# Kernel tuning notes

Measured on AMD Instinct MI355X. Metric: run time of the kernel, lower is better.

Reference implementation:

```python
import jax, jax.numpy as jnp
import numpy as np

N = 20000          # nodes
E = 320000         # edges (avg degree 16)
HID = 256          # hidden_size
HEADS = 8          # num_heads
HD = HID // HEADS  # head_dim = 32


def setup_inputs() -> dict:
    key = jax.random.key(0)
    ks = jax.random.split(key, 12)
    scale = 1.0 / np.sqrt(HID).astype(np.float32)
    def lin_w(k):
        return jax.random.normal(k, (HID, HID), jnp.float32) * scale
    def lin_b(k):
        return jax.random.normal(k, (HID,), jnp.float32) * 0.01
    return {
        "h":   jax.random.normal(ks[0], (N, HID), jnp.float32),
        "Wq": lin_w(ks[1]), "bq": lin_b(ks[2]),
        "Wk": lin_w(ks[3]), "bk": lin_b(ks[4]),
        "Wv": lin_w(ks[5]), "bv": lin_b(ks[6]),
        "Wo": lin_w(ks[7]), "bo": lin_b(ks[8]),
        "rows": jax.random.randint(ks[9],  (E,), 0, N),  # dst/query node of each edge
        "cols": jax.random.randint(ks[10], (E,), 0, N),  # src/key node of each edge
    }


def reference(h, Wq, bq, Wk, bk, Wv, bv, Wo, bo, rows, cols):
    n = h.shape[0]
    scaling = HD ** (-0.5)
    # projections; reshape exactly as torch: (N, head_dim, num_heads)
    q = ((h @ Wq) + bq).reshape(n, HD, HEADS) * scaling
    k = ((h @ Wk) + bk).reshape(n, HD, HEADS)
    v = ((h @ Wv) + bv).reshape(n, HD, HEADS)
    # bsddmm: per-edge, per-head score s[e,h] = sum_d q[rows[e],d,h] * k[cols[e],d,h]
    s = jnp.einsum("edh,edh->eh", q[rows], k[cols])  # [E, HEADS]
    # sparse row-wise softmax (over each row's edges)
    m = jax.ops.segment_max(s, rows, num_segments=n)          # [N, HEADS]
    e = jnp.exp(s - m[rows])                                   # [E, HEADS]
    z = jax.ops.segment_sum(e, rows, num_segments=n)           # [N, HEADS]
    attn = e / z[rows]                                          # [E, HEADS]
    # bspmm: out[i,d,h] = sum_{e: rows[e]=i} attn[e,h] * v[cols[e],d,h]
    out = jax.ops.segment_sum(attn[:, None, :] * v[cols], rows, num_segments=n)  # [N, HD, HEADS]
    return out.reshape(n, -1) @ Wo + bo
```

## Files before the change

kernel.cpp:

```cpp
#include <hip/hip_runtime.h>
#include <hip/hip_bf16.h>
#include <math.h>

#define NNODES 20000
#define NEDGES 320000

using f32x4 = __attribute__((ext_vector_type(4))) float;
using s16x8 = __attribute__((ext_vector_type(8))) short;
using u16x8 = __attribute__((ext_vector_type(8))) unsigned short;

__device__ __forceinline__ float bf2f(unsigned short u) {
    union { unsigned int i; float f; } c; c.i = ((unsigned int)u) << 16; return c.f;
}
__device__ __forceinline__ unsigned short f2bf(float f) {
    __hip_bfloat16 h = __float2bfloat16(f);
    return *reinterpret_cast<unsigned short*>(&h);
}

__global__ __launch_bounds__(256) void prep_hist_k(
    const float* __restrict__ Wq, const float* __restrict__ bq,
    const float* __restrict__ Wk, const float* __restrict__ bk,
    const float* __restrict__ Wv, const float* __restrict__ bv,
    const float* __restrict__ Wo, const int* __restrict__ rows,
    unsigned short* __restrict__ wt, float* __restrict__ bp,
    int* __restrict__ counts)
{
    const int gid = blockIdx.x * 256 + threadIdx.x;
    const float SC = 0.17677669529663687f;
    if (gid < 262144) {
        const int mat = gid >> 16, r = gid & 65535;
        if (mat < 3) {
            const int k = r >> 8, c = r & 255;
            const int n_old = ((c & 31) << 3) | (c >> 5);
            const float* W = (mat == 0) ? Wq : (mat == 1) ? Wk : Wv;
            float val = W[k * 256 + n_old];
            if (mat == 0) val *= SC;
            wt[mat * 65536 + c * 256 + k] = f2bf(val);
        } else {
            const int c = r >> 8, n = r & 255;
            const int n_old = ((c & 31) << 3) | (c >> 5);
            wt[3 * 65536 + n * 256 + c] = f2bf(Wo[n_old * 256 + n]);
        }
    } else if (gid < 262912) {
        const int idx = gid - 262144;
        const int mat = idx >> 8, c = idx & 255;
        const int n_old = ((c & 31) << 3) | (c >> 5);
        const float* b = (mat == 0) ? bq : (mat == 1) ? bk : bv;
        float val = b[n_old];
        if (mat == 0) val *= SC;
        bp[mat * 256 + c] = val;
    } else if (gid < 262912 + NEDGES) {
        atomicAdd(&counts[rows[gid - 262912]], 1);
    }
}

__global__ __launch_bounds__(1024) void scan_k(const int* __restrict__ counts,
                                               int* __restrict__ row_start)
{
    __shared__ int wsum[16];
    __shared__ int s_carry;
    const int t = threadIdx.x, lane = t & 63, w = t >> 6;
    if (t == 0) { s_carry = 0; row_start[0] = 0; }
    __syncthreads();
    for (int base = 0; base < NNODES; base += 4096) {
        int c[4]; int s4 = 0;
        #pragma unroll
        for (int j = 0; j < 4; ++j) {
            const int idx = base + t * 4 + j;
            c[j] = (idx < NNODES) ? counts[idx] : 0;
            s4 += c[j];
        }
        int incl = s4;
        #pragma unroll
        for (int off = 1; off < 64; off <<= 1) {
            const int y = __shfl_up(incl, off);
            if (lane >= off) incl += y;
        }
        if (lane == 63) wsum[w] = incl;
        __syncthreads();
        int prev = 0;
        for (int i = 0; i < w; ++i) prev += wsum[i];
        int total = 0;
        #pragma unroll
        for (int i = 0; i < 16; ++i) total += wsum[i];
        int run = s_carry + prev + incl - s4;
        #pragma unroll
        for (int j = 0; j < 4; ++j) {
            const int idx = base + t * 4 + j;
            run += c[j];
            if (idx < NNODES) row_start[idx + 1] = run;
        }
        __syncthreads();
        if (t == 0) s_carry += total;
        __syncthreads();
    }
}

__global__ void scatter_k(const int* __restrict__ rows, const int* __restrict__ cols,
                          const int* __restrict__ row_start, int* __restrict__ cursor,
                          int* __restrict__ cols_sorted)
{
    const int i = blockIdx.x * blockDim.x + threadIdx.x;
    if (i < NEDGES) {
        const int r = rows[i];
        const int pos = row_start[r] + atomicAdd(&cursor[r], 1);
        cols_sorted[pos] = cols[i];
    }
}

__global__ __launch_bounds__(256) void qkv_mfma_k(
    const float* __restrict__ h,
    const unsigned short* __restrict__ wt, const float* __restrict__ bp,
    unsigned short* __restrict__ qo, unsigned short* __restrict__ kv)
{
    const int bm = blockIdx.x * 128;
    const int mat = blockIdx.y >> 1;
    const int bn = (blockIdx.y & 1) * 128;
    const unsigned short* W = wt + mat * 65536;
    const float* bias = bp + mat * 256;

    __shared__ __align__(16) unsigned short As[128][40];
    __shared__ __align__(16) unsigned short Bs[128][40];

    const int t = threadIdx.x;
    const int lane = t & 63, w = t >> 6;
    const int wr = (w >> 1) * 64, wc = (w & 1) * 64;

    f32x4 acc[4][4];
    #pragma unroll
    for (int i = 0; i < 4; ++i)
        #pragma unroll
        for (int j = 0; j < 4; ++j) acc[i][j] = (f32x4){0.f, 0.f, 0.f, 0.f};

    const int srow = t >> 2, koff = (t & 3) * 8;
    for (int kt = 0; kt < 8; ++kt) {
        const int k0 = kt * 32;
        const int m0 = min(bm + srow, NNODES - 1);
        const int m1 = min(bm + srow + 64, NNODES - 1);
        {
            const float4 fa = *reinterpret_cast<const float4*>(&h[m0 * 256 + k0 + koff]);
            const float4 fb = *reinterpret_cast<const float4*>(&h[m0 * 256 + k0 + koff + 4]);
            u16x8 u; u[0]=f2bf(fa.x); u[1]=f2bf(fa.y); u[2]=f2bf(fa.z); u[3]=f2bf(fa.w);
                     u[4]=f2bf(fb.x); u[5]=f2bf(fb.y); u[6]=f2bf(fb.z); u[7]=f2bf(fb.w);
            *reinterpret_cast<u16x8*>(&As[srow][koff]) = u;
        }
        {
            const float4 fa = *reinterpret_cast<const float4*>(&h[m1 * 256 + k0 + koff]);
            const float4 fb = *reinterpret_cast<const float4*>(&h[m1 * 256 + k0 + koff + 4]);
            u16x8 u; u[0]=f2bf(fa.x); u[1]=f2bf(fa.y); u[2]=f2bf(fa.z); u[3]=f2bf(fa.w);
                     u[4]=f2bf(fb.x); u[5]=f2bf(fb.y); u[6]=f2bf(fb.z); u[7]=f2bf(fb.w);
            *reinterpret_cast<u16x8*>(&As[srow + 64][koff]) = u;
        }
        *reinterpret_cast<u16x8*>(&Bs[srow][koff]) =
            *reinterpret_cast<const u16x8*>(&W[(bn + srow) * 256 + k0 + koff]);
        *reinterpret_cast<u16x8*>(&Bs[srow + 64][koff]) =
            *reinterpret_cast<const u16x8*>(&W[(bn + srow + 64) * 256 + k0 + koff]);
        __syncthreads();
        s16x8 a[4], b[4];
        const int kk = (lane >> 4) * 8;
        #pragma unroll
        for (int i = 0; i < 4; ++i) {
            a[i] = *reinterpret_cast<const s16x8*>(&As[wr + i * 16 + (lane & 15)][kk]);
            b[i] = *reinterpret_cast<const s16x8*>(&Bs[wc + i * 16 + (lane & 15)][kk]);
        }
        #pragma unroll
        for (int i = 0; i < 4; ++i)
            #pragma unroll
            for (int j = 0; j < 4; ++j)
                acc[i][j] = __builtin_amdgcn_mfma_f32_16x16x32_bf16(a[i], b[j], acc[i][j], 0, 0, 0);
        __syncthreads();
    }
    #pragma unroll
    for (int i = 0; i < 4; ++i)
        #pragma unroll
        for (int j = 0; j < 4; ++j) {
            const int n = bn + wc + j * 16 + (lane & 15);
            const float bval = bias[n];
            const int kvbase = ((n >> 2) << 3) + (n & 3) + ((mat == 2) ? 4 : 0);
            #pragma unroll
            for (int r = 0; r < 4; ++r) {
                const int m = bm + wr + i * 16 + (lane >> 4) * 4 + r;
                if (m < NNODES) {
                    const unsigned short val = f2bf(acc[i][j][r] + bval);
                    if (mat == 0) qo[m * 256 + n] = val;
                    else          kv[m * 512 + kvbase] = val;
                }
            }
        }
}

__global__ __launch_bounds__(256) void out_mfma_k(
    const unsigned short* __restrict__ A,
    const unsigned short* __restrict__ wt, const float* __restrict__ bo,
    float* __restrict__ C)
{
    const int bm = blockIdx.x * 128;
    const int bn = blockIdx.y * 128;
    const unsigned short* W = wt + 3 * 65536;

    __shared__ __align__(16) unsigned short As[128][40];
    __shared__ __align__(16) unsigned short Bs[128][40];

    const int t = threadIdx.x;
    const int lane = t & 63, w = t >> 6;
    const int wr = (w >> 1) * 64, wc = (w & 1) * 64;

    f32x4 acc[4][4];
    #pragma unroll
    for (int i = 0; i < 4; ++i)
        #pragma unroll
        for (int j = 0; j < 4; ++j) acc[i][j] = (f32x4){0.f, 0.f, 0.f, 0.f};

    const int srow = t >> 2, koff = (t & 3) * 8;
    for (int kt = 0; kt < 8; ++kt) {
        const int k0 = kt * 32;
        const int m0 = min(bm + srow, NNODES - 1);
        const int m1 = min(bm + srow + 64, NNODES - 1);
        *reinterpret_cast<u16x8*>(&As[srow][koff]) =
            *reinterpret_cast<const u16x8*>(&A[m0 * 256 + k0 + koff]);
        *reinterpret_cast<u16x8*>(&As[srow + 64][koff]) =
            *reinterpret_cast<const u16x8*>(&A[m1 * 256 + k0 + koff]);
        *reinterpret_cast<u16x8*>(&Bs[srow][koff]) =
            *reinterpret_cast<const u16x8*>(&W[(bn + srow) * 256 + k0 + koff]);
        *reinterpret_cast<u16x8*>(&Bs[srow + 64][koff]) =
            *reinterpret_cast<const u16x8*>(&W[(bn + srow + 64) * 256 + k0 + koff]);
        __syncthreads();
        s16x8 a[4], b[4];
        const int kk = (lane >> 4) * 8;
        #pragma unroll
        for (int i = 0; i < 4; ++i) {
            a[i] = *reinterpret_cast<const s16x8*>(&As[wr + i * 16 + (lane & 15)][kk]);
            b[i] = *reinterpret_cast<const s16x8*>(&Bs[wc + i * 16 + (lane & 15)][kk]);
        }
        #pragma unroll
        for (int i = 0; i < 4; ++i)
            #pragma unroll
            for (int j = 0; j < 4; ++j)
                acc[i][j] = __builtin_amdgcn_mfma_f32_16x16x32_bf16(a[i], b[j], acc[i][j], 0, 0, 0);
        __syncthreads();
    }
    #pragma unroll
    for (int i = 0; i < 4; ++i)
        #pragma unroll
        for (int j = 0; j < 4; ++j) {
            const int n = bn + wc + j * 16 + (lane & 15);
            const float bval = bo[n];
            #pragma unroll
            for (int r = 0; r < 4; ++r) {
                const int m = bm + wr + i * 16 + (lane >> 4) * 4 + r;
                if (m < NNODES) C[m * 256 + n] = acc[i][j][r] + bval;
            }
        }
}

__global__ __launch_bounds__(256) void row_attn_k(
    const unsigned short* __restrict__ q, const unsigned short* __restrict__ kv,
    const int* __restrict__ row_start, const int* __restrict__ cols_sorted,
    unsigned short* __restrict__ ot)
{
    const int lane = threadIdx.x & 63;
    const int row = blockIdx.x * 4 + (threadIdx.x >> 6);
    if (row >= NNODES) return;
    const int rs = row_start[row], re = row_start[row + 1];

    const ushort4 qu = *reinterpret_cast<const ushort4*>(&q[row * 256 + lane * 4]);
    const float q0 = bf2f(qu.x), q1 = bf2f(qu.y), q2 = bf2f(qu.z), q3 = bf2f(qu.w);
    float z = 0.f, o0 = 0.f, o1 = 0.f, o2 = 0.f, o3 = 0.f;

    for (int c0 = rs; c0 < re; c0 += 64) {
        const int nch = min(64, re - c0);
        const int cn_reg = (c0 + lane < re) ? cols_sorted[c0 + lane] : 0;
        #pragma unroll 4
        for (int i = 0; i < nch; ++i) {
            const int cn = __shfl(cn_reg, i);
            const u16x8 kv8 = *reinterpret_cast<const u16x8*>(&kv[cn * 512 + lane * 8]);
            float p = q0 * bf2f(kv8[0]);
            p = fmaf(q1, bf2f(kv8[1]), p);
            p = fmaf(q2, bf2f(kv8[2]), p);
            p = fmaf(q3, bf2f(kv8[3]), p);
            p += __shfl_xor(p, 1);
            p += __shfl_xor(p, 2);
            p += __shfl_xor(p, 4);
            const float e = __expf(p);
            z += e;
            o0 = fmaf(e, bf2f(kv8[4]), o0);
            o1 = fmaf(e, bf2f(kv8[5]), o1);
            o2 = fmaf(e, bf2f(kv8[6]), o2);
            o3 = fmaf(e, bf2f(kv8[7]), o3);
        }
    }
    ushort4 r;
    if (re > rs) {
        const float iz = 1.0f / z;
        r.x = f2bf(o0 * iz); r.y = f2bf(o1 * iz);
        r.z = f2bf(o2 * iz); r.w = f2bf(o3 * iz);
    } else {
        r.x = r.y = r.z = r.w = 0;
    }
    *reinterpret_cast<ushort4*>(&ot[row * 256 + lane * 4]) = r;
}

extern "C" void kernel_launch(void* const* d_in, const int* in_sizes, int n_in,
                              void* d_out, int out_size, void* d_ws, size_t ws_size,
                              hipStream_t stream)
{
    const float* h  = (const float*)d_in[0];
    const float* Wq = (const float*)d_in[1];
    const float* bq = (const float*)d_in[2];
    const float* Wk = (const float*)d_in[3];
    const float* bk = (const float*)d_in[4];
    const float* Wv = (const float*)d_in[5];
    const float* bv = (const float*)d_in[6];
    const float* Wo = (const float*)d_in[7];
    const float* bo = (const float*)d_in[8];
    const int* rows = (const int*)d_in[9];
    const int* cols = (const int*)d_in[10];
    float* outp = (float*)d_out;

    char* ws = (char*)d_ws;
    unsigned short* q_b  = (unsigned short*)(ws + 0);
    unsigned short* kv_b = (unsigned short*)(ws + 10240000);
    unsigned short* ot_b = (unsigned short*)(ws + 30720000);
    unsigned short* wt   = (unsigned short*)(ws + 40960000);
    float* bp            = (float*)(ws + 41484288);
    int* row_start       = (int*)(ws + 41487360);
    int* counts          = (int*)(ws + 41567488);
    int* cursor          = (int*)(ws + 41647488);
    int* cols_sorted     = (int*)(ws + 41727488);

    hipMemsetAsync(ws + 41567488, 0, 160000, stream);

    prep_hist_k<<<2277, 256, 0, stream>>>(Wq, bq, Wk, bk, Wv, bv, Wo, rows,
                                          wt, bp, counts);
    scan_k<<<1, 1024, 0, stream>>>(counts, row_start);
    scatter_k<<<1250, 256, 0, stream>>>(rows, cols, row_start, cursor, cols_sorted);
    qkv_mfma_k<<<dim3(157, 6), 256, 0, stream>>>(h, wt, bp, q_b, kv_b);
    row_attn_k<<<5000, 256, 0, stream>>>(q_b, kv_b, row_start, cols_sorted, ot_b);
    out_mfma_k<<<dim3(157, 2), 256, 0, stream>>>(ot_b, wt, bo, outp);
}
```

Measured before the change: 231.8 us.

## Double-buffer GEMM tiles, batch edge gathers in attention, single-pass scan

Both MFMA GEMM kernels now use double-buffered shared-memory tiles and prefetch the next K-slice into registers while the current slice is being multiplied, so global load latency overlaps with compute. The row-attention kernel issues eight kv gathers at once per batch, reading column indices straight from memory, which raises memory-level parallelism on the random gathers. Masking handles the tail of each batch. The scan kernel replaces the looped 4-element passes with one pass of 20 elements per thread. Costs are higher register and LDS use per block, which could lower occupancy. The removed row bounds check depends on the grid exactly covering NNODES (20000/4 divides evenly).

```diff
diff --git a/kernel.cpp b/kernel.cpp
--- a/kernel.cpp
+++ b/kernel.cpp
@@ -15,6 +15,11 @@
 __device__ __forceinline__ unsigned short f2bf(float f) {
     __hip_bfloat16 h = __float2bfloat16(f);
     return *reinterpret_cast<unsigned short*>(&h);
+}
+__device__ __forceinline__ u16x8 packA(const float4& x, const float4& y) {
+    u16x8 u; u[0]=f2bf(x.x); u[1]=f2bf(x.y); u[2]=f2bf(x.z); u[3]=f2bf(x.w);
+             u[4]=f2bf(y.x); u[5]=f2bf(y.y); u[6]=f2bf(y.z); u[7]=f2bf(y.w);
+    return u;
 }
 
 __global__ __launch_bounds__(256) void prep_hist_k(
@@ -58,41 +63,32 @@
                                                int* __restrict__ row_start)
 {
     __shared__ int wsum[16];
-    __shared__ int s_carry;
     const int t = threadIdx.x, lane = t & 63, w = t >> 6;
-    if (t == 0) { s_carry = 0; row_start[0] = 0; }
+    const int base = t * 20;
+    int c[20]; int s = 0;
+    #pragma unroll
+    for (int j = 0; j < 20; ++j) {
+        const int idx = base + j;
+        c[j] = (idx < NNODES) ? counts[idx] : 0;
+        s += c[j];
+    }
+    int incl = s;
+    #pragma unroll
+    for (int off = 1; off < 64; off <<= 1) {
+        const int y = __shfl_up(incl, off);
+        if (lane >= off) incl += y;
+    }
+    if (lane == 63) wsum[w] = incl;
     __syncthreads();
-    for (int base = 0; base < NNODES; base += 4096) {
-        int c[4]; int s4 = 0;
-        #pragma unroll
-        for (int j = 0; j < 4; ++j) {
-            const int idx = base + t * 4 + j;
-            c[j] = (idx < NNODES) ? counts[idx] : 0;
-            s4 += c[j];
-        }
-        int incl = s4;
-        #pragma unroll
-        for (int off = 1; off < 64; off <<= 1) {
-            const int y = __shfl_up(incl, off);
-            if (lane >= off) incl += y;
-        }
-        if (lane == 63) wsum[w] = incl;
-        __syncthreads();
-        int prev = 0;
-        for (int i = 0; i < w; ++i) prev += wsum[i];
-        int total = 0;
-        #pragma unroll
-        for (int i = 0; i < 16; ++i) total += wsum[i];
-        int run = s_carry + prev + incl - s4;
-        #pragma unroll
-        for (int j = 0; j < 4; ++j) {
-            const int idx = base + t * 4 + j;
-            run += c[j];
-            if (idx < NNODES) row_start[idx + 1] = run;
-        }
-        __syncthreads();
-        if (t == 0) s_carry += total;
-        __syncthreads();
+    int prev = 0;
+    for (int i = 0; i < w; ++i) prev += wsum[i];
+    int run = prev + incl - s;
+    if (t == 0) row_start[0] = 0;
+    #pragma unroll
+    for (int j = 0; j < 20; ++j) {
+        const int idx = base + j;
+        run += c[j];
+        if (idx < NNODES) row_start[idx + 1] = run;
     }
 }
 
@@ -119,8 +115,8 @@
     const unsigned short* W = wt + mat * 65536;
     const float* bias = bp + mat * 256;
 
-    __shared__ __align__(16) unsigned short As[128][40];
-    __shared__ __align__(16) unsigned short Bs[128][40];
+    __shared__ __align__(16) unsigned short As[2][128][40];
+    __shared__ __align__(16) unsigned short Bs[2][128][40];
 
     const int t = threadIdx.x;
     const int lane = t & 63, w = t >> 6;
@@ -133,42 +129,52 @@
         for (int j = 0; j < 4; ++j) acc[i][j] = (f32x4){0.f, 0.f, 0.f, 0.f};
 
     const int srow = t >> 2, koff = (t & 3) * 8;
+    const int m0 = min(bm + srow, NNODES - 1);
+    const int m1 = min(bm + srow + 64, NNODES - 1);
+    const float* pa0 = h + m0 * 256 + koff;
+    const float* pa1 = h + m1 * 256 + koff;
+    const unsigned short* pb0 = W + (bn + srow) * 256 + koff;
+    const unsigned short* pb1 = W + (bn + srow + 64) * 256 + koff;
+
+    float4 fa0a = *(const float4*)(pa0), fa0b = *(const float4*)(pa0 + 4);
+    float4 fa1a = *(const float4*)(pa1), fa1b = *(const float4*)(pa1 + 4);
+    u16x8 rb0 = *(const u16x8*)(pb0), rb1 = *(const u16x8*)(pb1);
+
+    *(u16x8*)&As[0][srow][koff]      = packA(fa0a, fa0b);
+    *(u16x8*)&As[0][srow + 64][koff] = packA(fa1a, fa1b);
+    *(u16x8*)&Bs[0][srow][koff]      = rb0;
+    *(u16x8*)&Bs[0][srow + 64][koff] = rb1;
+    __syncthreads();
+
+    #pragma unroll
     for (int kt = 0; kt < 8; ++kt) {
-        const int k0 = kt * 32;
-        const int m0 = min(bm + srow, NNODES - 1);
-        const int m1 = min(bm + srow + 64, NNODES - 1);
-        {
-            const float4 fa = *reinterpret_cast<const float4*>(&h[m0 * 256 + k0 + koff]);
-            const float4 fb = *reinterpret_cast<const float4*>(&h[m0 * 256 + k0 + koff + 4]);
-            u16x8 u; u[0]=f2bf(fa.x); u[1]=f2bf(fa.y); u[2]=f2bf(fa.z); u[3]=f2bf(fa.w);
-                     u[4]=f2bf(fb.x); u[5]=f2bf(fb.y); u[6]=f2bf(fb.z); u[7]=f2bf(fb.w);
-            *reinterpret_cast<u16x8*>(&As[srow][koff]) = u;
-        }
-        {
-            const float4 fa = *reinterpret_cast<const float4*>(&h[m1 * 256 + k0 + koff]);
-            const float4 fb = *reinterpret_cast<const float4*>(&h[m1 * 256 + k0 + koff + 4]);
-            u16x8 u; u[0]=f2bf(fa.x); u[1]=f2bf(fa.y); u[2]=f2bf(fa.z); u[3]=f2bf(fa.w);
-                     u[4]=f2bf(fb.x); u[5]=f2bf(fb.y); u[6]=f2bf(fb.z); u[7]=f2bf(fb.w);
-            *reinterpret_cast<u16x8*>(&As[srow + 64][koff]) = u;
-        }
-        *reinterpret_cast<u16x8*>(&Bs[srow][koff]) =
-            *reinterpret_cast<const u16x8*>(&W[(bn + srow) * 256 + k0 + koff]);
-        *reinterpret_cast<u16x8*>(&Bs[srow + 64][koff]) =
-            *reinterpret_cast<const u16x8*>(&W[(bn + srow + 64) * 256 + k0 + koff]);
-        __syncthreads();
+        const int cur = kt & 1;
+        if (kt < 7) {
+            const int k0 = (kt + 1) * 32;
+            fa0a = *(const float4*)(pa0 + k0); fa0b = *(const float4*)(pa0 + k0 + 4);
+            fa1a = *(const float4*)(pa1 + k0); fa1b = *(const float4*)(pa1 + k0 + 4);
+            rb0 = *(const u16x8*)(pb0 + k0);   rb1 = *(const u16x8*)(pb1 + k0);
+        }
         s16x8 a[4], b[4];
         const int kk = (lane >> 4) * 8;
         #pragma unroll
         for (int i = 0; i < 4; ++i) {
-            a[i] = *reinterpret_cast<const s16x8*>(&As[wr + i * 16 + (lane & 15)][kk]);
-            b[i] = *reinterpret_cast<const s16x8*>(&Bs[wc + i * 16 + (lane & 15)][kk]);
+            a[i] = *(const s16x8*)&As[cur][wr + i * 16 + (lane & 15)][kk];
+            b[i] = *(const s16x8*)&Bs[cur][wc + i * 16 + (lane & 15)][kk];
         }
         #pragma unroll
         for (int i = 0; i < 4; ++i)
             #pragma unroll
             for (int j = 0; j < 4; ++j)
                 acc[i][j] = __builtin_amdgcn_mfma_f32_16x16x32_bf16(a[i], b[j], acc[i][j], 0, 0, 0);
-        __syncthreads();
+        if (kt < 7) {
+            __syncthreads();
+            *(u16x8*)&As[cur ^ 1][srow][koff]      = packA(fa0a, fa0b);
+            *(u16x8*)&As[cur ^ 1][srow + 64][koff] = packA(fa1a, fa1b);
+            *(u16x8*)&Bs[cur ^ 1][srow][koff]      = rb0;
+            *(u16x8*)&Bs[cur ^ 1][srow + 64][koff] = rb1;
+            __syncthreads();
+        }
     }
     #pragma unroll
     for (int i = 0; i < 4; ++i)
@@ -198,8 +204,8 @@
     const int bn = blockIdx.y * 128;
     const unsigned short* W = wt + 3 * 65536;
 
-    __shared__ __align__(16) unsigned short As[128][40];
-    __shared__ __align__(16) unsigned short Bs[128][40];
+    __shared__ __align__(16) unsigned short As[2][128][40];
+    __shared__ __align__(16) unsigned short Bs[2][128][40];
 
     const int t = threadIdx.x;
     const int lane = t & 63, w = t >> 6;
@@ -212,32 +218,50 @@
         for (int j = 0; j < 4; ++j) acc[i][j] = (f32x4){0.f, 0.f, 0.f, 0.f};
 
     const int srow = t >> 2, koff = (t & 3) * 8;
+    const int m0 = min(bm + srow, NNODES - 1);
+    const int m1 = min(bm + srow + 64, NNODES - 1);
+    const unsigned short* pa0 = A + m0 * 256 + koff;
+    const unsigned short* pa1 = A + m1 * 256 + koff;
+    const unsigned short* pb0 = W + (bn + srow) * 256 + koff;
+    const unsigned short* pb1 = W + (bn + srow + 64) * 256 + koff;
+
+    u16x8 ra0 = *(const u16x8*)(pa0), ra1 = *(const u16x8*)(pa1);
+    u16x8 rb0 = *(const u16x8*)(pb0), rb1 = *(const u16x8*)(pb1);
+
+    *(u16x8*)&As[0][srow][koff]      = ra0;
+    *(u16x8*)&As[0][srow + 64][koff] = ra1;
+    *(u16x8*)&Bs[0][srow][koff]      = rb0;
+    *(u16x8*)&Bs[0][srow + 64][koff] = rb1;
+    __syncthreads();
+
+    #pragma unroll
     for (int kt = 0; kt < 8; ++kt) {
-        const int k0 = kt * 32;
-        const int m0 = min(bm + srow, NNODES - 1);
-        const int m1 = min(bm + srow + 64, NNODES - 1);
-        *reinterpret_cast<u16x8*>(&As[srow][koff]) =
-            *reinterpret_cast<const u16x8*>(&A[m0 * 256 + k0 + koff]);
-        *reinterpret_cast<u16x8*>(&As[srow + 64][koff]) =
-            *reinterpret_cast<const u16x8*>(&A[m1 * 256 + k0 + koff]);
-        *reinterpret_cast<u16x8*>(&Bs[srow][koff]) =
-            *reinterpret_cast<const u16x8*>(&W[(bn + srow) * 256 + k0 + koff]);
-        *reinterpret_cast<u16x8*>(&Bs[srow + 64][koff]) =
-            *reinterpret_cast<const u16x8*>(&W[(bn + srow + 64) * 256 + k0 + koff]);
-        __syncthreads();
+        const int cur = kt & 1;
+        if (kt < 7) {
+            const int k0 = (kt + 1) * 32;
+            ra0 = *(const u16x8*)(pa0 + k0); ra1 = *(const u16x8*)(pa1 + k0);
+            rb0 = *(const u16x8*)(pb0 + k0); rb1 = *(const u16x8*)(pb1 + k0);
+        }
         s16x8 a[4], b[4];
         const int kk = (lane >> 4) * 8;
         #pragma unroll
         for (int i = 0; i < 4; ++i) {
-            a[i] = *reinterpret_cast<const s16x8*>(&As[wr + i * 16 + (lane & 15)][kk]);
-            b[i] = *reinterpret_cast<const s16x8*>(&Bs[wc + i * 16 + (lane & 15)][kk]);
+            a[i] = *(const s16x8*)&As[cur][wr + i * 16 + (lane & 15)][kk];
+            b[i] = *(const s16x8*)&Bs[cur][wc + i * 16 + (lane & 15)][kk];
         }
         #pragma unroll
         for (int i = 0; i < 4; ++i)
             #pragma unroll
             for (int j = 0; j < 4; ++j)
                 acc[i][j] = __builtin_amdgcn_mfma_f32_16x16x32_bf16(a[i], b[j], acc[i][j], 0, 0, 0);
-        __syncthreads();
+        if (kt < 7) {
+            __syncthreads();
+            *(u16x8*)&As[cur ^ 1][srow][koff]      = ra0;
+            *(u16x8*)&As[cur ^ 1][srow + 64][koff] = ra1;
+            *(u16x8*)&Bs[cur ^ 1][srow][koff]      = rb0;
+            *(u16x8*)&Bs[cur ^ 1][srow + 64][koff] = rb1;
+            __syncthreads();
+        }
     }
     #pragma unroll
     for (int i = 0; i < 4; ++i)
@@ -259,38 +283,43 @@
     unsigned short* __restrict__ ot)
 {
     const int lane = threadIdx.x & 63;
-    const int row = blockIdx.x * 4 + (threadIdx.x >> 6);
-    if (row >= NNODES) return;
-    const int rs = row_start[row], re = row_start[row + 1];
+    const int row = __builtin_amdgcn_readfirstlane(blockIdx.x * 4 + (threadIdx.x >> 6));
+    const int rs = row_start[row];
+    const int re = row_start[row + 1];
+    const int deg = re - rs;
 
     const ushort4 qu = *reinterpret_cast<const ushort4*>(&q[row * 256 + lane * 4]);
     const float q0 = bf2f(qu.x), q1 = bf2f(qu.y), q2 = bf2f(qu.z), q3 = bf2f(qu.w);
     float z = 0.f, o0 = 0.f, o1 = 0.f, o2 = 0.f, o3 = 0.f;
 
-    for (int c0 = rs; c0 < re; c0 += 64) {
-        const int nch = min(64, re - c0);
-        const int cn_reg = (c0 + lane < re) ? cols_sorted[c0 + lane] : 0;
-        #pragma unroll 4
-        for (int i = 0; i < nch; ++i) {
-            const int cn = __shfl(cn_reg, i);
-            const u16x8 kv8 = *reinterpret_cast<const u16x8*>(&kv[cn * 512 + lane * 8]);
-            float p = q0 * bf2f(kv8[0]);
-            p = fmaf(q1, bf2f(kv8[1]), p);
-            p = fmaf(q2, bf2f(kv8[2]), p);
-            p = fmaf(q3, bf2f(kv8[3]), p);
+    const int* cp = cols_sorted + rs;
+    for (int i0 = 0; i0 < deg; i0 += 8) {
+        u16x8 kvb[8];
+        #pragma unroll
+        for (int j = 0; j < 8; ++j) {
+            const int jj = min(i0 + j, deg - 1);
+            const int cn = cp[jj];
+            kvb[j] = *reinterpret_cast<const u16x8*>(&kv[cn * 512 + lane * 8]);
+        }
+        #pragma unroll
+        for (int j = 0; j < 8; ++j) {
+            float p = q0 * bf2f(kvb[j][0]);
+            p = fmaf(q1, bf2f(kvb[j][1]), p);
+            p = fmaf(q2, bf2f(kvb[j][2]), p);
+            p = fmaf(q3, bf2f(kvb[j][3]), p);
             p += __shfl_xor(p, 1);
             p += __shfl_xor(p, 2);
             p += __shfl_xor(p, 4);
-            const float e = __expf(p);
+            const float e = (i0 + j < deg) ? __expf(p) : 0.f;
             z += e;
-            o0 = fmaf(e, bf2f(kv8[4]), o0);
-            o1 = fmaf(e, bf2f(kv8[5]), o1);
-            o2 = fmaf(e, bf2f(kv8[6]), o2);
-            o3 = fmaf(e, bf2f(kv8[7]), o3);
+            o0 = fmaf(e, bf2f(kvb[j][4]), o0);
+            o1 = fmaf(e, bf2f(kvb[j][5]), o1);
+            o2 = fmaf(e, bf2f(kvb[j][6]), o2);
+            o3 = fmaf(e, bf2f(kvb[j][7]), o3);
         }
     }
     ushort4 r;
-    if (re > rs) {
+    if (deg > 0) {
         const float iz = 1.0f / z;
         r.x = f2bf(o0 * iz); r.y = f2bf(o1 * iz);
         r.z = f2bf(o2 * iz); r.w = f2bf(o3 * iz);
```

Measured after the change: 233.2 us. About the same (+0.6%).
